# Performance work log

Measured on AMD Instinct MI355X. Metric: run time of the kernel, lower is better.

## Reference

```python
import jax, jax.numpy as jnp
from jax import lax
import numpy as np

SCORE_THRESH = 0.05
NMS_THRESH = 0.5
MAX_DET = 100
MIN_SIZE = 0.01
BBOX_CLIP = float(np.log(1000.0 / 16.0))
NEG = -1e10


def setup_inputs() -> dict:
    key = jax.random.key(0)
    ks = jax.random.split(key, 12)
    N, IN, REP, C = 2000, 256 * 7 * 7, 1024, 91
    box_features = jax.random.normal(ks[0], (N, IN), jnp.float32)
    x1 = jax.random.uniform(ks[1], (N,), jnp.float32, 0.0, 1000.0)
    y1 = jax.random.uniform(ks[2], (N,), jnp.float32, 0.0, 600.0)
    bw = jax.random.uniform(ks[3], (N,), jnp.float32, 16.0, 200.0)
    bh = jax.random.uniform(ks[4], (N,), jnp.float32, 16.0, 180.0)
    proposals = jnp.stack([x1, y1, x1 + bw, y1 + bh], axis=1)
    W1 = jax.random.normal(ks[5], (IN, REP), jnp.float32) * 0.01
    b1 = jnp.zeros((REP,), jnp.float32)
    W2 = jax.random.normal(ks[6], (REP, REP), jnp.float32) * 0.03
    b2 = jnp.zeros((REP,), jnp.float32)
    Wc = jax.random.normal(ks[7], (REP, C), jnp.float32) * 0.1
    bc = jax.random.normal(ks[8], (C,), jnp.float32) * 0.5
    Wr = jax.random.normal(ks[9], (REP, 4 * C), jnp.float32) * 0.01
    br = jnp.zeros((4 * C,), jnp.float32)
    return dict(box_features=box_features, proposals=proposals,
                W1=W1, b1=b1, W2=W2, b2=b2, Wc=Wc, bc=bc, Wr=Wr, br=br,
                image_h=800, image_w=1216)


def _nms(boxes, scores):
    """Greedy NMS with fixed trip count; scores already masked to NEG for invalid."""
    M = boxes.shape[0]
    areas = (boxes[:, 2] - boxes[:, 0]) * (boxes[:, 3] - boxes[:, 1])
    idxs = jnp.arange(M)

    def step(sm, _):
        i = jnp.argmax(sm)
        valid = sm[i] > NEG * 0.5
        b = boxes[i]
        xx1 = jnp.maximum(b[0], boxes[:, 0]); yy1 = jnp.maximum(b[1], boxes[:, 1])
        xx2 = jnp.minimum(b[2], boxes[:, 2]); yy2 = jnp.minimum(b[3], boxes[:, 3])
        inter = jnp.clip(xx2 - xx1, 0.0) * jnp.clip(yy2 - yy1, 0.0)
        iou = inter / (areas[i] + areas - inter + 1e-9)
        suppress = (iou > NMS_THRESH) | (idxs == i)
        sm = jnp.where(valid, jnp.where(suppress, NEG, sm), sm)
        return sm, jnp.where(valid, i, -1)

    _, keep = lax.scan(step, scores, None, length=MAX_DET)
    return keep  # [MAX_DET] int, -1 for padding


def reference(box_features, proposals, W1, b1, W2, b2, Wc, bc, Wr, br, image_h, image_w):
    N = box_features.shape[0]
    C = Wc.shape[1]
    # box head MLP (Linear+ReLU x2) and predictors
    h = jax.nn.relu(box_features @ W1 + b1)
    h = jax.nn.relu(h @ W2 + b2)
    class_logits = h @ Wc + bc                      # [N, C]
    box_reg = (h @ Wr + br).reshape(N, C, 4)        # [N, C, 4]
    # box decode (weights 10,10,5,5) against proposals
    pw = proposals[:, 2] - proposals[:, 0]
    ph = proposals[:, 3] - proposals[:, 1]
    pcx = proposals[:, 0] + 0.5 * pw
    pcy = proposals[:, 1] + 0.5 * ph
    dx = box_reg[..., 0] / 10.0
    dy = box_reg[..., 1] / 10.0
    dw = jnp.minimum(box_reg[..., 2] / 5.0, BBOX_CLIP)
    dh = jnp.minimum(box_reg[..., 3] / 5.0, BBOX_CLIP)
    cx = dx * pw[:, None] + pcx[:, None]
    cy = dy * ph[:, None] + pcy[:, None]
    w = jnp.exp(dw) * pw[:, None]
    hh = jnp.exp(dh) * ph[:, None]
    boxes = jnp.stack([cx - 0.5 * w, cy - 0.5 * hh, cx + 0.5 * w, cy + 0.5 * hh], axis=-1)
    scores = jax.nn.softmax(class_logits, axis=-1)
    # clip to image
    Wim = jnp.float32(image_w); Him = jnp.float32(image_h)
    boxes = jnp.stack([jnp.clip(boxes[..., 0], 0.0, Wim),
                       jnp.clip(boxes[..., 1], 0.0, Him),
                       jnp.clip(boxes[..., 2], 0.0, Wim),
                       jnp.clip(boxes[..., 3], 0.0, Him)], axis=-1)
    # drop background class, flatten to [N*(C-1)]
    boxes = boxes[:, 1:].reshape(-1, 4)
    scores = scores[:, 1:].reshape(-1)
    labels = jnp.broadcast_to(jnp.arange(1, C, dtype=jnp.int32), (N, C - 1)).reshape(-1)
    # score threshold + remove small boxes (as masking, static shapes)
    bw = boxes[:, 2] - boxes[:, 0]
    bh = boxes[:, 3] - boxes[:, 1]
    valid = (scores > SCORE_THRESH) & (bw >= MIN_SIZE) & (bh >= MIN_SIZE)
    sm = jnp.where(valid, scores, NEG)
    # class-aware (batched) NMS via per-class coordinate offsets
    off = labels.astype(boxes.dtype) * (jnp.maximum(Wim, Him) + 1.0)
    keep = _nms(boxes + off[:, None], sm)
    mask = keep >= 0
    idx = jnp.maximum(keep, 0)
    out_boxes = jnp.take(boxes, idx, axis=0) * mask[:, None]
    out_scores = jnp.take(scores, idx) * mask
    out_labels = jnp.take(labels, idx) * mask.astype(jnp.int32)
    return out_boxes, out_scores, out_labels
```

## Files before the change

kernel.cpp:

```cpp
#include <hip/hip_runtime.h>

#define CPC 2000
#define SPC 100
#define NCLS 90
#define TM 128
#define TN 128
#define TKK 16

typedef __attribute__((ext_vector_type(8))) short bf16x8;
typedef __attribute__((ext_vector_type(4))) float f32x4;
typedef __attribute__((ext_vector_type(4))) unsigned short u16x4;

__device__ __forceinline__ unsigned short f2bf_rne(float f) {
    unsigned u = __float_as_uint(f);
    return (unsigned short)((u + 0x7FFFu + ((u >> 16) & 1u)) >> 16);
}
__device__ __forceinline__ unsigned short f2bf_trunc(float f) {
    return (unsigned short)(__float_as_uint(f) >> 16);
}
__device__ __forceinline__ float bfhi_f32(float f) {
    return __uint_as_float(__float_as_uint(f) & 0xFFFF0000u);
}
__device__ __forceinline__ void async_load16(const void* g, void* l) {
    __builtin_amdgcn_global_load_lds((const __attribute__((address_space(1))) unsigned int*)g,
                                     (__attribute__((address_space(3))) unsigned int*)l, 16, 0, 0);
}
__device__ __forceinline__ int swz(int c) { return c ^ ((c >> 3) & 3); }

__global__ __launch_bounds__(256) void split_transpose(
    const float* __restrict__ W, unsigned short* __restrict__ Thi,
    unsigned short* __restrict__ Tlo, int K, int N)
{
    __shared__ float tile[64][33];
    const int kt = blockIdx.x * 64, nt = blockIdx.y * 32;
    const int tx = threadIdx.x & 31, ty = threadIdx.x >> 5;
#pragma unroll
    for (int j = 0; j < 8; ++j) {
        int k = kt + ty + j * 8, n = nt + tx;
        tile[ty + j * 8][tx] = (k < K && n < N) ? W[(size_t)k * N + n] : 0.f;
    }
    __syncthreads();
#pragma unroll
    for (int j = 0; j < 4; ++j) {
        int n = nt + ty + j * 8;
        int k = kt + tx * 2;
        if (n < N && k < K) {
            float f0 = tile[tx * 2][ty + j * 8];
            float f1 = tile[tx * 2 + 1][ty + j * 8];
            unsigned hi = (unsigned)f2bf_trunc(f0) | ((unsigned)f2bf_trunc(f1) << 16);
            unsigned lo = (unsigned)f2bf_rne(f0 - bfhi_f32(f0))
                        | ((unsigned)f2bf_rne(f1 - bfhi_f32(f1)) << 16);
            *reinterpret_cast<unsigned*>(&Thi[(size_t)n * K + k]) = hi;
            *reinterpret_cast<unsigned*>(&Tlo[(size_t)n * K + k]) = lo;
        }
    }
}

__global__ __launch_bounds__(256) void split_transpose2(
    const float* __restrict__ Wa, const float* __restrict__ Wb, int Na, int Nb,
    unsigned short* __restrict__ Thi, unsigned short* __restrict__ Tlo, int K)
{
    const int N = Na + Nb;
    __shared__ float tile[64][33];
    const int kt = blockIdx.x * 64, nt = blockIdx.y * 32;
    const int tx = threadIdx.x & 31, ty = threadIdx.x >> 5;
#pragma unroll
    for (int j = 0; j < 8; ++j) {
        int k = kt + ty + j * 8, n = nt + tx;
        float v = 0.f;
        if (k < K && n < N)
            v = (n < Na) ? Wa[(size_t)k * Na + n] : Wb[(size_t)k * Nb + (n - Na)];
        tile[ty + j * 8][tx] = v;
    }
    __syncthreads();
#pragma unroll
    for (int j = 0; j < 4; ++j) {
        int n = nt + ty + j * 8;
        int k = kt + tx * 2;
        if (n < N && k < K) {
            float f0 = tile[tx * 2][ty + j * 8];
            float f1 = tile[tx * 2 + 1][ty + j * 8];
            unsigned hi = (unsigned)f2bf_trunc(f0) | ((unsigned)f2bf_trunc(f1) << 16);
            unsigned lo = (unsigned)f2bf_rne(f0 - bfhi_f32(f0))
                        | ((unsigned)f2bf_rne(f1 - bfhi_f32(f1)) << 16);
            *reinterpret_cast<unsigned*>(&Thi[(size_t)n * K + k]) = hi;
            *reinterpret_cast<unsigned*>(&Tlo[(size_t)n * K + k]) = lo;
        }
    }
}

__global__ __launch_bounds__(256, 6) void gemm_bf16x3_f32a(
    const float* __restrict__ A, const unsigned short* __restrict__ Bhi,
    const unsigned short* __restrict__ Blo, float* __restrict__ C,
    int M, int N, int K, int klen)
{
    __shared__ unsigned short Ah[2048], Al[2048], Bh[4096], Bl[4096];
    const int tid = threadIdx.x;
    const int wv = tid >> 6, ln = tid & 63;
    const int q = ln >> 4, lm = ln & 15;
    const int m0 = blockIdx.y * 64, n0 = blockIdx.x * 128;
    const int k0 = blockIdx.z * klen;
    int k1 = k0 + klen; if (k1 > K) k1 = K;
    const int bcol_t = wv * 32;

    f32x4 acc[4][2];
#pragma unroll
    for (int i = 0; i < 4; ++i)
#pragma unroll
        for (int j = 0; j < 2; ++j) acc[i][j] = (f32x4)0.f;

    int gr = m0 + (tid >> 2); if (gr >= M) gr = M - 1;
    const float* Arow = A + (size_t)gr * K + (tid & 3) * 8;
    const int apc = swz(tid);

    unsigned bsrc[2];
#pragma unroll
    for (int i = 0; i < 2; ++i) {
        int s = i * 256 + tid;
        int gn = n0 + (s >> 2); if (gn >= N) gn = N - 1;
        int qe = (s & 3) ^ ((s >> 3) & 3);
        bsrc[i] = (unsigned)gn * (unsigned)K + (unsigned)(qe * 8);
    }

    for (int kt = k0; kt < k1; kt += 32) {
#pragma unroll
        for (int i = 0; i < 2; ++i) {
            async_load16(Bhi + bsrc[i] + kt, &Bh[(i * 256 + wv * 64) * 8]);
            async_load16(Blo + bsrc[i] + kt, &Bl[(i * 256 + wv * 64) * 8]);
        }
        float4 v0 = *reinterpret_cast<const float4*>(Arow + kt);
        float4 v1 = *reinterpret_cast<const float4*>(Arow + kt + 4);
        float f[8] = {v0.x, v0.y, v0.z, v0.w, v1.x, v1.y, v1.z, v1.w};
        bf16x8 hi, lo;
#pragma unroll
        for (int e = 0; e < 8; ++e) {
            hi[e] = (short)f2bf_trunc(f[e]);
            lo[e] = (short)f2bf_rne(f[e] - bfhi_f32(f[e]));
        }
        *(bf16x8*)&Ah[apc * 8] = hi;
        *(bf16x8*)&Al[apc * 8] = lo;
        __syncthreads();

        bf16x8 afh[4], afl[4], bfh[2], bfl[2];
#pragma unroll
        for (int mi = 0; mi < 4; ++mi) {
            int p = swz((mi * 16 + lm) * 4 + q);
            afh[mi] = *(const bf16x8*)&Ah[p * 8];
            afl[mi] = *(const bf16x8*)&Al[p * 8];
        }
#pragma unroll
        for (int ni = 0; ni < 2; ++ni) {
            int p = swz((bcol_t + ni * 16 + lm) * 4 + q);
            bfh[ni] = *(const bf16x8*)&Bh[p * 8];
            bfl[ni] = *(const bf16x8*)&Bl[p * 8];
        }
#pragma unroll
        for (int mi = 0; mi < 4; ++mi)
#pragma unroll
            for (int ni = 0; ni < 2; ++ni) {
                acc[mi][ni] = __builtin_amdgcn_mfma_f32_16x16x32_bf16(afh[mi], bfh[ni], acc[mi][ni], 0, 0, 0);
                acc[mi][ni] = __builtin_amdgcn_mfma_f32_16x16x32_bf16(afl[mi], bfh[ni], acc[mi][ni], 0, 0, 0);
                acc[mi][ni] = __builtin_amdgcn_mfma_f32_16x16x32_bf16(afh[mi], bfl[ni], acc[mi][ni], 0, 0, 0);
            }
        __syncthreads();
    }

    float* Cz = C + (size_t)blockIdx.z * (size_t)M * (size_t)N;
#pragma unroll
    for (int mi = 0; mi < 4; ++mi)
#pragma unroll
        for (int ni = 0; ni < 2; ++ni)
#pragma unroll
            for (int ri = 0; ri < 4; ++ri) {
                int rr = m0 + mi * 16 + q * 4 + ri;
                int cc = n0 + bcol_t + ni * 16 + lm;
                if (rr < M && cc < N) Cz[(size_t)rr * N + cc] = acc[mi][ni][ri];
            }
}

__global__ __launch_bounds__(256, 6) void gemm_bf16x3_sa(
    const unsigned short* __restrict__ Ahi_g, const unsigned short* __restrict__ Alo_g,
    const unsigned short* __restrict__ Bhi, const unsigned short* __restrict__ Blo,
    float* __restrict__ C, int M, int N, int K, int klen)
{
    __shared__ unsigned short Ah[2048], Al[2048], Bh[4096], Bl[4096];
    const int tid = threadIdx.x;
    const int wv = tid >> 6, ln = tid & 63;
    const int q = ln >> 4, lm = ln & 15;
    const int m0 = blockIdx.y * 64, n0 = blockIdx.x * 128;
    const int k0 = blockIdx.z * klen;
    int k1 = k0 + klen; if (k1 > K) k1 = K;
    const int bcol_t = wv * 32;

    f32x4 acc[4][2];
#pragma unroll
    for (int i = 0; i < 4; ++i)
#pragma unroll
        for (int j = 0; j < 2; ++j) acc[i][j] = (f32x4)0.f;

    int agr = m0 + (tid >> 2); if (agr >= M) agr = M - 1;
    const unsigned asrc = (unsigned)agr * (unsigned)K
                        + (unsigned)(((tid & 3) ^ ((tid >> 3) & 3)) * 8);

    unsigned bsrc[2];
#pragma unroll
    for (int i = 0; i < 2; ++i) {
        int s = i * 256 + tid;
        int gn = n0 + (s >> 2); if (gn >= N) gn = N - 1;
        int qe = (s & 3) ^ ((s >> 3) & 3);
        bsrc[i] = (unsigned)gn * (unsigned)K + (unsigned)(qe * 8);
    }

    for (int kt = k0; kt < k1; kt += 32) {
        async_load16(Ahi_g + asrc + kt, &Ah[(wv * 64) * 8]);
        async_load16(Alo_g + asrc + kt, &Al[(wv * 64) * 8]);
#pragma unroll
        for (int i = 0; i < 2; ++i) {
            async_load16(Bhi + bsrc[i] + kt, &Bh[(i * 256 + wv * 64) * 8]);
            async_load16(Blo + bsrc[i] + kt, &Bl[(i * 256 + wv * 64) * 8]);
        }
        __syncthreads();

        bf16x8 afh[4], afl[4], bfh[2], bfl[2];
#pragma unroll
        for (int mi = 0; mi < 4; ++mi) {
            int p = swz((mi * 16 + lm) * 4 + q);
            afh[mi] = *(const bf16x8*)&Ah[p * 8];
            afl[mi] = *(const bf16x8*)&Al[p * 8];
        }
#pragma unroll
        for (int ni = 0; ni < 2; ++ni) {
            int p = swz((bcol_t + ni * 16 + lm) * 4 + q);
            bfh[ni] = *(const bf16x8*)&Bh[p * 8];
            bfl[ni] = *(const bf16x8*)&Bl[p * 8];
        }
#pragma unroll
        for (int mi = 0; mi < 4; ++mi)
#pragma unroll
            for (int ni = 0; ni < 2; ++ni) {
                acc[mi][ni] = __builtin_amdgcn_mfma_f32_16x16x32_bf16(afh[mi], bfh[ni], acc[mi][ni], 0, 0, 0);
                acc[mi][ni] = __builtin_amdgcn_mfma_f32_16x16x32_bf16(afl[mi], bfh[ni], acc[mi][ni], 0, 0, 0);
                acc[mi][ni] = __builtin_amdgcn_mfma_f32_16x16x32_bf16(afh[mi], bfl[ni], acc[mi][ni], 0, 0, 0);
            }
        __syncthreads();
    }

    float* Cz = C + (size_t)blockIdx.z * (size_t)M * (size_t)N;
#pragma unroll
    for (int mi = 0; mi < 4; ++mi)
#pragma unroll
        for (int ni = 0; ni < 2; ++ni)
#pragma unroll
            for (int ri = 0; ri < 4; ++ri) {
                int rr = m0 + mi * 16 + q * 4 + ri;
                int cc = n0 + bcol_t + ni * 16 + lm;
                if (rr < M && cc < N) Cz[(size_t)rr * N + cc] = acc[mi][ni][ri];
            }
}

__global__ __launch_bounds__(256) void gemm_f32(
    const float* __restrict__ A, const float* __restrict__ B,
    const float* __restrict__ bias, float* __restrict__ C,
    int M, int N, int K, int ksplit, int relu)
{
    __shared__ float As[TKK][TM + 4];
    __shared__ float Bs[TKK][TN + 4];
    const int tid = threadIdx.x;
    const int tx = tid & 15, ty = tid >> 4;
    const int m0 = blockIdx.y * TM, n0 = blockIdx.x * TN;
    const int z = blockIdx.z;
    const int kstart = z * ksplit;
    const int kend = (kstart + ksplit < K) ? (kstart + ksplit) : K;
    float* Cz = C + (size_t)z * (size_t)M * (size_t)N;
    const bool nvec = ((N & 3) == 0);

    float acc[8][8];
#pragma unroll
    for (int i = 0; i < 8; ++i)
#pragma unroll
        for (int j = 0; j < 8; ++j) acc[i][j] = 0.f;

    for (int kt = kstart; kt < kend; kt += TKK) {
#pragma unroll
        for (int l = 0; l < 2; ++l) {
            int idx = tid + l * 256;
            int rr = idx >> 2, kq = idx & 3;
            float4 v = make_float4(0.f, 0.f, 0.f, 0.f);
            int grr = m0 + rr;
            if (grr < M)
                v = *reinterpret_cast<const float4*>(A + (size_t)grr * K + kt + (kq << 2));
            As[(kq << 2) + 0][rr] = v.x;
            As[(kq << 2) + 1][rr] = v.y;
            As[(kq << 2) + 2][rr] = v.z;
            As[(kq << 2) + 3][rr] = v.w;
        }
#pragma unroll
        for (int l = 0; l < 2; ++l) {
            int idx = tid + l * 256;
            int kk = idx >> 5, nq = idx & 31;
            int gn = n0 + (nq << 2);
            const float* bp = B + (size_t)(kt + kk) * N + gn;
            float4 v;
            if (nvec && gn + 3 < N) {
                v = *reinterpret_cast<const float4*>(bp);
            } else {
                v.x = (gn + 0 < N) ? bp[0] : 0.f;
                v.y = (gn + 1 < N) ? bp[1] : 0.f;
                v.z = (gn + 2 < N) ? bp[2] : 0.f;
                v.w = (gn + 3 < N) ? bp[3] : 0.f;
            }
            *reinterpret_cast<float4*>(&Bs[kk][nq << 2]) = v;
        }
        __syncthreads();
#pragma unroll
        for (int kk = 0; kk < TKK; ++kk) {
            float a[8], b[8];
            *reinterpret_cast<float4*>(&a[0]) = *reinterpret_cast<const float4*>(&As[kk][ty * 8]);
            *reinterpret_cast<float4*>(&a[4]) = *reinterpret_cast<const float4*>(&As[kk][ty * 8 + 4]);
            *reinterpret_cast<float4*>(&b[0]) = *reinterpret_cast<const float4*>(&Bs[kk][tx * 4]);
            *reinterpret_cast<float4*>(&b[4]) = *reinterpret_cast<const float4*>(&Bs[kk][64 + tx * 4]);
#pragma unroll
            for (int i = 0; i < 8; ++i)
#pragma unroll
                for (int j = 0; j < 8; ++j)
                    acc[i][j] = fmaf(a[i], b[j], acc[i][j]);
        }
        __syncthreads();
    }
#pragma unroll
    for (int i = 0; i < 8; ++i) {
        int grr = m0 + ty * 8 + i;
        if (grr >= M) continue;
#pragma unroll
        for (int j = 0; j < 8; ++j) {
            int gc = n0 + ((j < 4) ? (tx * 4 + j) : (64 + tx * 4 + (j - 4)));
            if (gc >= N) continue;
            float v = acc[i][j];
            if (bias) v += bias[gc];
            if (relu) v = fmaxf(v, 0.f);
            Cz[(size_t)grr * N + gc] = v;
        }
    }
}

__global__ void combine_bias_act(const float* __restrict__ P, const float* __restrict__ bias,
                                 float* __restrict__ H, int total, int N, int nsplit,
                                 int pstride, int relu)
{
    int i = blockIdx.x * blockDim.x + threadIdx.x;
    if (i >= total) return;
    float s = P[i];
    for (int j = 1; j < nsplit; ++j) s += P[i + (size_t)j * (size_t)pstride];
    s += bias[i % N];
    if (relu) s = fmaxf(s, 0.f);
    H[i] = s;
}

__global__ void combine_bias_split(const float* __restrict__ P, const float* __restrict__ bias,
                                   unsigned short* __restrict__ Hhi, unsigned short* __restrict__ Hlo,
                                   int total, int N, int nsplit, int pstride, int relu)
{
    int i = (blockIdx.x * blockDim.x + threadIdx.x) * 4;
    if (i >= total) return;
    float4 s = *reinterpret_cast<const float4*>(P + i);
    for (int j = 1; j < nsplit; ++j) {
        float4 p = *reinterpret_cast<const float4*>(P + i + (size_t)j * (size_t)pstride);
        s.x += p.x; s.y += p.y; s.z += p.z; s.w += p.w;
    }
    const float4 b = *reinterpret_cast<const float4*>(bias + (i % N));
    s.x += b.x; s.y += b.y; s.z += b.z; s.w += b.w;
    if (relu) {
        s.x = fmaxf(s.x, 0.f); s.y = fmaxf(s.y, 0.f);
        s.z = fmaxf(s.z, 0.f); s.w = fmaxf(s.w, 0.f);
    }
    u16x4 hi = { f2bf_trunc(s.x), f2bf_trunc(s.y), f2bf_trunc(s.z), f2bf_trunc(s.w) };
    u16x4 lo = { f2bf_rne(s.x - bfhi_f32(s.x)), f2bf_rne(s.y - bfhi_f32(s.y)),
                 f2bf_rne(s.z - bfhi_f32(s.z)), f2bf_rne(s.w - bfhi_f32(s.w)) };
    *reinterpret_cast<u16x4*>(&Hhi[i]) = hi;
    *reinterpret_cast<u16x4*>(&Hlo[i]) = lo;
}

__global__ void combine_head(const float* __restrict__ P, const float* __restrict__ bc,
                             const float* __restrict__ br, float* __restrict__ H,
                             int total, int nsplit, int pstride)
{
    int i = (blockIdx.x * blockDim.x + threadIdx.x) * 4;
    if (i >= total) return;
    float4 s = *reinterpret_cast<const float4*>(P + i);
    for (int j = 1; j < nsplit; ++j) {
        float4 p = *reinterpret_cast<const float4*>(P + i + (size_t)j * (size_t)pstride);
        s.x += p.x; s.y += p.y; s.z += p.z; s.w += p.w;
    }
    float sv[4] = {s.x, s.y, s.z, s.w};
#pragma unroll
    for (int e = 0; e < 4; ++e) {
        int col = (i + e) % 455;
        sv[e] += (col < 91) ? bc[col] : br[col - 91];
    }
    *reinterpret_cast<float4*>(&H[i]) = make_float4(sv[0], sv[1], sv[2], sv[3]);
}

__device__ __forceinline__ float scalar_dim(const int* p)
{
    int iv = *p;
    return (iv > 0 && iv < (1 << 20)) ? (float)iv : *reinterpret_cast<const float*>(p);
}

__global__ __launch_bounds__(128) void decode_compact(
    const float* __restrict__ logits, int lstr, const float* __restrict__ breg, int bstr,
    const float4* __restrict__ proposals, const int* __restrict__ ihp,
    const int* __restrict__ iwp,
    float4* __restrict__ cbox, float* __restrict__ cscore, int* __restrict__ cn,
    int* __restrict__ ccnt)
{
    const int n = blockIdx.x;
    const int c = threadIdx.x;
    __shared__ float sl[91];
    __shared__ float red[128];
    if (c < 91) sl[c] = logits[(size_t)n * lstr + c];
    __syncthreads();
    red[c] = (c < 91) ? sl[c] : -3.0e38f;
    __syncthreads();
#pragma unroll
    for (int s = 64; s > 0; s >>= 1) {
        if (c < s) red[c] = fmaxf(red[c], red[c + s]);
        __syncthreads();
    }
    const float s_max = red[0];
    __syncthreads();
    red[c] = (c < 91) ? expf(sl[c] - s_max) : 0.f;
    __syncthreads();
#pragma unroll
    for (int s = 64; s > 0; s >>= 1) {
        if (c < s) red[c] += red[c + s];
        __syncthreads();
    }
    const float s_sum = red[0];
    if (c < 1 || c >= 91) return;

    const float score = expf(sl[c] - s_max) / s_sum;
    const float Wim = scalar_dim(iwp), Him = scalar_dim(ihp);
    float4 p = proposals[n];
    float pw = p.z - p.x, ph = p.w - p.y;
    float pcx = p.x + 0.5f * pw, pcy = p.y + 0.5f * ph;
    const float* r4 = breg + (size_t)n * bstr + c * 4;
    float dxv = r4[0] / 10.f, dyv = r4[1] / 10.f;
    const float BCLIP = 4.135166556742356f;
    float dwv = fminf(r4[2] / 5.f, BCLIP);
    float dhv = fminf(r4[3] / 5.f, BCLIP);
    float cx = dxv * pw + pcx, cy = dyv * ph + pcy;
    float w = expf(dwv) * pw, hh = expf(dhv) * ph;
    float x1 = cx - 0.5f * w, y1 = cy - 0.5f * hh;
    float x2 = cx + 0.5f * w, y2 = cy + 0.5f * hh;
    x1 = fminf(fmaxf(x1, 0.f), Wim);
    y1 = fminf(fmaxf(y1, 0.f), Him);
    x2 = fminf(fmaxf(x2, 0.f), Wim);
    y2 = fminf(fmaxf(y2, 0.f), Him);
    float bw = x2 - x1, bh = y2 - y1;
    if (score > 0.05f && bw >= 0.01f && bh >= 0.01f) {
        int cls = c - 1;
        int pos = atomicAdd(&ccnt[cls], 1);
        if (pos < CPC) {
            cbox[cls * CPC + pos] = make_float4(x1, y1, x2, y2);
            cscore[cls * CPC + pos] = score;
            cn[cls * CPC + pos] = n;
        }
    }
}

__global__ __launch_bounds__(256) void nms_class(
    const float4* __restrict__ cbox, const float* __restrict__ cscore,
    const int* __restrict__ cn, const int* __restrict__ ccnt,
    float4* __restrict__ sbox, float* __restrict__ sscore,
    unsigned long long* __restrict__ skey, int* __restrict__ scnt)
{
    const int cls = blockIdx.x;
    const int tid = threadIdx.x;
    int cnt = ccnt[cls]; if (cnt > CPC) cnt = CPC;

    __shared__ float4 cb[CPC];
    __shared__ unsigned long long keys[CPC];
    __shared__ unsigned long long red[4];
    __shared__ float4 selsh;
    __shared__ int selidx_sh;

    for (int i = tid; i < cnt; i += 256) {
        cb[i] = cbox[cls * CPC + i];
        unsigned int sb = __float_as_uint(cscore[cls * CPC + i]);
        sb ^= (sb >> 31) ? 0xFFFFFFFFu : 0x80000000u;
        unsigned int flat = (unsigned)cn[cls * CPC + i] * 90u + (unsigned)cls;
        keys[i] = ((unsigned long long)sb << 32) | (unsigned long long)(0xFFFFFFFFu - flat);
    }
    __syncthreads();

    int sel = 0;
    while (sel < SPC) {
        unsigned long long best = 0ull;
        for (int i = tid; i < cnt; i += 256) {
            unsigned long long k = keys[i];
            if (k > best) best = k;
        }
#pragma unroll
        for (int d = 32; d >= 1; d >>= 1) {
            unsigned long long o = __shfl_down(best, d, 64);
            if (o > best) best = o;
        }
        if ((tid & 63) == 0) red[tid >> 6] = best;
        __syncthreads();
        unsigned long long gbest = red[0];
        if (red[1] > gbest) gbest = red[1];
        if (red[2] > gbest) gbest = red[2];
        if (red[3] > gbest) gbest = red[3];
        if (gbest == 0ull) break;
        for (int i = tid; i < cnt; i += 256)
            if (keys[i] == gbest) { selsh = cb[i]; selidx_sh = i; }
        __syncthreads();
        float4 s = selsh;
        const int si = selidx_sh;
        const float sa = (s.z - s.x) * (s.w - s.y);
        if (tid == 0) {
            sbox[cls * SPC + sel] = s;
            unsigned int sb = (unsigned int)(gbest >> 32);
            sb ^= (sb >> 31) ? 0x80000000u : 0xFFFFFFFFu;
            sscore[cls * SPC + sel] = __uint_as_float(sb);
            skey[cls * SPC + sel] = gbest;
        }
        for (int i = tid; i < cnt; i += 256) {
            float4 b = cb[i];
            float xx1 = fmaxf(s.x, b.x), yy1 = fmaxf(s.y, b.y);
            float xx2 = fminf(s.z, b.z), yy2 = fminf(s.w, b.w);
            float inter = fmaxf(xx2 - xx1, 0.f) * fmaxf(yy2 - yy1, 0.f);
            float area = (b.z - b.x) * (b.w - b.y);
            if (3.f * inter > sa + area + 1e-9f || i == si) keys[i] = 0ull;
        }
        ++sel;
        __syncthreads();
    }
    if (tid == 0) scnt[cls] = sel;
}

__global__ __launch_bounds__(128) void nms_merge(
    const float4* __restrict__ sbox, const float* __restrict__ sscore,
    const unsigned long long* __restrict__ skey, const int* __restrict__ scnt,
    float* __restrict__ out)
{
    const int tid = threadIdx.x;
    __shared__ int head[NCLS];
    __shared__ unsigned long long red[2];
    __shared__ int selc_sh;
    if (tid < NCLS) head[tid] = 0;
    __syncthreads();

    for (int k = 0; k < 100; ++k) {
        unsigned long long key = 0ull;
        if (tid < NCLS && head[tid] < scnt[tid]) key = skey[tid * SPC + head[tid]];
        unsigned long long mykey = key;
#pragma unroll
        for (int d = 32; d >= 1; d >>= 1) {
            unsigned long long o = __shfl_down(key, d, 64);
            if (o > key) key = o;
        }
        if ((tid & 63) == 0) red[tid >> 6] = key;
        if (tid == 0) selc_sh = -1;
        __syncthreads();
        unsigned long long gbest = red[0] > red[1] ? red[0] : red[1];
        if (gbest != 0ull && mykey == gbest) selc_sh = tid;
        __syncthreads();
        const int c = selc_sh;
        if (tid == 0) {
            if (c >= 0) {
                int h = head[c];
                float4 b = sbox[c * SPC + h];
                out[k * 4 + 0] = b.x; out[k * 4 + 1] = b.y;
                out[k * 4 + 2] = b.z; out[k * 4 + 3] = b.w;
                out[400 + k] = sscore[c * SPC + h];
                out[500 + k] = (float)(c + 1);
            } else {
                out[k * 4 + 0] = 0.f; out[k * 4 + 1] = 0.f;
                out[k * 4 + 2] = 0.f; out[k * 4 + 3] = 0.f;
                out[400 + k] = 0.f; out[500 + k] = 0.f;
            }
        }
        if (c >= 0 && tid == c) head[c]++;
        __syncthreads();
    }
}

extern "C" void kernel_launch(void* const* d_in, const int* in_sizes, int n_in,
                              void* d_out, int out_size, void* d_ws, size_t ws_size,
                              hipStream_t stream)
{
    const float* bf    = (const float*)d_in[0];
    const float* props = (const float*)d_in[1];
    const float* W1    = (const float*)d_in[2];
    const float* b1    = (const float*)d_in[3];
    const float* W2    = (const float*)d_in[4];
    const float* b2    = (const float*)d_in[5];
    const float* Wc    = (const float*)d_in[6];
    const float* bc    = (const float*)d_in[7];
    const float* Wr    = (const float*)d_in[8];
    const float* br    = (const float*)d_in[9];
    const int*   ihp   = (const int*)d_in[10];
    const int*   iwp   = (const int*)d_in[11];
    float* ws  = (float*)d_ws;
    float* out = (float*)d_out;

    const size_t MN   = 2000ull * 1024ull;
    const size_t NLOG = 2000ull * 91ull;
    const size_t NREG = 2000ull * 364ull;
    const size_t NHEAD = 2000ull * 455ull;
    const size_t ws_floats = ws_size / 4;

    const size_t BT1F = 1024ull * 12544ull / 2;
    const size_t WT2F = 1024ull * 1024ull / 2;
    const size_t WHF  = 455ull * 1024ull / 2;
    const size_t NMSF = (size_t)NCLS * CPC * 6 + (size_t)NCLS * SPC * 7 + 256;
    const size_t PF   = 4 * MN;
    const size_t NEED = 2 * BT1F + 2 * WT2F + 2 * WHF + 2 * MN + NHEAD + NMSF + PF + 64;

    if (ws_floats >= NEED) {
        unsigned short* BT1hi = (unsigned short*)ws;
        unsigned short* BT1lo = (unsigned short*)(ws + BT1F);
        unsigned short* WT2hi = (unsigned short*)(ws + 2 * BT1F);
        unsigned short* WT2lo = (unsigned short*)(ws + 2 * BT1F + WT2F);
        unsigned short* WHhi  = (unsigned short*)(ws + 2 * BT1F + 2 * WT2F);
        unsigned short* WHlo  = (unsigned short*)(ws + 2 * BT1F + 2 * WT2F + WHF);
        float* T = ws + 2 * BT1F + 2 * WT2F + 2 * WHF;

        float* H1   = T;
        float* P1   = T + MN;
        float* P2   = T + MN;
        float* H2   = T + 6 * MN;
        float* P3   = T;
        float* HEAD = T + 7 * MN;
        float* CBOX   = T;
        float* CSCORE = CBOX + (size_t)NCLS * CPC * 4;
        int*   CN     = (int*)(CSCORE + (size_t)NCLS * CPC);
        float* SBOX   = (float*)(CN + (size_t)NCLS * CPC);
        float* SSCORE = SBOX + (size_t)NCLS * SPC * 4;
        unsigned long long* SKEY = (unsigned long long*)(SSCORE + (size_t)NCLS * SPC);
        int*   CCNT = (int*)(SKEY + (size_t)NCLS * SPC);
        int*   SCNT = CCNT + NCLS;

        unsigned short* H1hi = (unsigned short*)H1;
        unsigned short* H1lo = H1hi + MN;
        unsigned short* H2hi = (unsigned short*)H2;
        unsigned short* H2lo = H2hi + MN;

        split_transpose<<<dim3(196, 32), 256, 0, stream>>>(W1, BT1hi, BT1lo, 12544, 1024);
        split_transpose<<<dim3(16, 32), 256, 0, stream>>>(W2, WT2hi, WT2lo, 1024, 1024);
        split_transpose2<<<dim3(16, 15), 256, 0, stream>>>(Wc, Wr, 91, 364, WHhi, WHlo, 1024);
        gemm_bf16x3_f32a<<<dim3(8, 32, 6), 256, 0, stream>>>(bf, BT1hi, BT1lo, P1,
                                                             2000, 1024, 12544, 2112);
        combine_bias_split<<<(int)(MN / 4 / 256), 256, 0, stream>>>(P1, b1, H1hi, H1lo,
                                                             (int)MN, 1024, 6, (int)MN, 1);
        gemm_bf16x3_sa<<<dim3(8, 32, 5), 256, 0, stream>>>(H1hi, H1lo, WT2hi, WT2lo, P2,
                                                           2000, 1024, 1024, 224);
        combine_bias_split<<<(int)(MN / 4 / 256), 256, 0, stream>>>(P2, b2, H2hi, H2lo,
                                                             (int)MN, 1024, 5, (int)MN, 1);
        gemm_bf16x3_sa<<<dim3(4, 32, 6), 256, 0, stream>>>(H2hi, H2lo, WHhi, WHlo, P3,
                                                           2000, 455, 1024, 192);
        combine_head<<<(int)((NHEAD / 4 + 255) / 256), 256, 0, stream>>>(P3, bc, br, HEAD,
                                                             (int)NHEAD, 6, (int)NHEAD);
        hipMemsetAsync(CCNT, 0, 2 * NCLS * sizeof(int), stream);
        decode_compact<<<2000, 128, 0, stream>>>(HEAD, 455, HEAD + 91, 455,
                                                 (const float4*)props, ihp, iwp,
                                                 (float4*)CBOX, CSCORE, CN, CCNT);
        nms_class<<<NCLS, 256, 0, stream>>>((const float4*)CBOX, CSCORE, CN, CCNT,
                                            (float4*)SBOX, SSCORE, SKEY, SCNT);
        nms_merge<<<1, 128, 0, stream>>>((const float4*)SBOX, SSCORE, SKEY, SCNT, out);
        return;
    }

    const size_t NMSF2 = (size_t)NCLS * CPC * 6 + (size_t)NCLS * SPC * 7 + 256;
    const size_t TAILF = 2 * MN + NLOG + NREG + NMSF2;
    int z1 = 2;
    if (ws_floats >= TAILF + 8 * MN) z1 = 8;
    else if (ws_floats >= TAILF + 4 * MN) z1 = 4;
    const size_t REUSE = (size_t)z1 * MN;
    int zh = (REUSE >= 8 * NREG) ? 8 : 4;

    float* P      = ws;
    float* H1     = P + REUSE;
    float* H2     = H1 + MN;
    float* LOG    = H2 + MN;
    float* BREG   = LOG + NLOG;
    float* CBOX   = BREG + NREG;
    float* CSCORE = CBOX + (size_t)NCLS * CPC * 4;
    int*   CN     = (int*)(CSCORE + (size_t)NCLS * CPC);
    float* SBOX   = (float*)(CN + (size_t)NCLS * CPC);
    float* SSCORE = SBOX + (size_t)NCLS * SPC * 4;
    unsigned long long* SKEY = (unsigned long long*)(SSCORE + (size_t)NCLS * SPC);
    int*   CCNT   = (int*)(SKEY + (size_t)NCLS * SPC);
    int*   SCNT   = CCNT + NCLS;

    gemm_f32<<<dim3(8, 16, z1), 256, 0, stream>>>(bf, W1, nullptr, P,
                                                  2000, 1024, 12544, 12544 / z1, 0);
    combine_bias_act<<<(int)((MN + 255) / 256), 256, 0, stream>>>(P, b1, H1,
                                                  (int)MN, 1024, z1, (int)MN, 1);
    gemm_f32<<<dim3(8, 16, 4), 256, 0, stream>>>(H1, W2, nullptr, P,
                                                 2000, 1024, 1024, 256, 0);
    combine_bias_act<<<(int)((MN + 255) / 256), 256, 0, stream>>>(P, b2, H2,
                                                 (int)MN, 1024, 4, (int)MN, 1);
    gemm_f32<<<dim3(1, 16, zh), 256, 0, stream>>>(H2, Wc, nullptr, P,
                                                  2000, 91, 1024, 1024 / zh, 0);
    combine_bias_act<<<(int)((NLOG + 255) / 256), 256, 0, stream>>>(P, bc, LOG,
                                                  (int)NLOG, 91, zh, (int)NLOG, 0);
    gemm_f32<<<dim3(3, 16, zh), 256, 0, stream>>>(H2, Wr, nullptr, P,
                                                  2000, 364, 1024, 1024 / zh, 0);
    combine_bias_act<<<(int)((NREG + 255) / 256), 256, 0, stream>>>(P, br, BREG,
                                                  (int)NREG, 364, zh, (int)NREG, 0);
    hipMemsetAsync(CCNT, 0, 2 * NCLS * sizeof(int), stream);
    decode_compact<<<2000, 128, 0, stream>>>(LOG, 91, BREG, 364,
                                             (const float4*)props, ihp, iwp,
                                             (float4*)CBOX, CSCORE, CN, CCNT);
    nms_class<<<NCLS, 256, 0, stream>>>((const float4*)CBOX, CSCORE, CN, CCNT,
                                        (float4*)SBOX, SSCORE, SKEY, SCNT);
    nms_merge<<<1, 128, 0, stream>>>((const float4*)SBOX, SSCORE, SKEY, SCNT, out);
}
```

Before: 830.6 us.

## Remap GEMM workgroups across XCDs, retune split-K, and separate partial-sum buffer

Adds an XCD-aware remap of linear block IDs so that neighbouring tiles, which share A and B panels, land on the same XCD and reuse its L2. It also lowers the launch-bounds occupancy hint from 6 to 4 and changes the split-K factors: 4 for the first two GEMMs and 8 for the head GEMM. The workspace is rearranged so partial sums go to a dedicated buffer P instead of aliasing the activation region. The aim is less L2 and HBM traffic in the large first GEMM and less partial-sum reduction work, at the cost of fewer blocks in flight for the first two GEMMs and a different register budget per block.

Measured after the change: 734.7 us. 1.13x faster.

```diff
diff --git a/kernel.cpp b/kernel.cpp
--- a/kernel.cpp
+++ b/kernel.cpp
@@ -26,6 +26,19 @@
                                      (__attribute__((address_space(3))) unsigned int*)l, 16, 0, 0);
 }
 __device__ __forceinline__ int swz(int c) { return c ^ ((c >> 3) & 3); }
+
+__device__ __forceinline__ void xcd_remap(unsigned& bx, unsigned& by, unsigned& bz)
+{
+    const unsigned nx = gridDim.x, ny = gridDim.y;
+    const unsigned nwg = nx * ny * gridDim.z;
+    unsigned lin = blockIdx.x + nx * (blockIdx.y + ny * blockIdx.z);
+    if ((nwg & 7u) == 0u)
+        lin = (lin & 7u) * (nwg >> 3) + (lin >> 3);
+    bx = lin % nx;
+    unsigned rem = lin / nx;
+    by = rem % ny;
+    bz = rem / ny;
+}
 
 __global__ __launch_bounds__(256) void split_transpose(
     const float* __restrict__ W, unsigned short* __restrict__ Thi,
@@ -89,17 +102,19 @@
     }
 }
 
-__global__ __launch_bounds__(256, 6) void gemm_bf16x3_f32a(
+__global__ __launch_bounds__(256, 4) void gemm_bf16x3_f32a(
     const float* __restrict__ A, const unsigned short* __restrict__ Bhi,
     const unsigned short* __restrict__ Blo, float* __restrict__ C,
     int M, int N, int K, int klen)
 {
     __shared__ unsigned short Ah[2048], Al[2048], Bh[4096], Bl[4096];
+    unsigned bxu, byu, bzu;
+    xcd_remap(bxu, byu, bzu);
     const int tid = threadIdx.x;
     const int wv = tid >> 6, ln = tid & 63;
     const int q = ln >> 4, lm = ln & 15;
-    const int m0 = blockIdx.y * 64, n0 = blockIdx.x * 128;
-    const int k0 = blockIdx.z * klen;
+    const int m0 = byu * 64, n0 = bxu * 128;
+    const int k0 = bzu * klen;
     int k1 = k0 + klen; if (k1 > K) k1 = K;
     const int bcol_t = wv * 32;
 
@@ -165,7 +180,7 @@
         __syncthreads();
     }
 
-    float* Cz = C + (size_t)blockIdx.z * (size_t)M * (size_t)N;
+    float* Cz = C + (size_t)bzu * (size_t)M * (size_t)N;
 #pragma unroll
     for (int mi = 0; mi < 4; ++mi)
 #pragma unroll
@@ -178,17 +193,19 @@
             }
 }
 
-__global__ __launch_bounds__(256, 6) void gemm_bf16x3_sa(
+__global__ __launch_bounds__(256, 4) void gemm_bf16x3_sa(
     const unsigned short* __restrict__ Ahi_g, const unsigned short* __restrict__ Alo_g,
     const unsigned short* __restrict__ Bhi, const unsigned short* __restrict__ Blo,
     float* __restrict__ C, int M, int N, int K, int klen)
 {
     __shared__ unsigned short Ah[2048], Al[2048], Bh[4096], Bl[4096];
+    unsigned bxu, byu, bzu;
+    xcd_remap(bxu, byu, bzu);
     const int tid = threadIdx.x;
     const int wv = tid >> 6, ln = tid & 63;
     const int q = ln >> 4, lm = ln & 15;
-    const int m0 = blockIdx.y * 64, n0 = blockIdx.x * 128;
-    const int k0 = blockIdx.z * klen;
+    const int m0 = byu * 64, n0 = bxu * 128;
+    const int k0 = bzu * klen;
     int k1 = k0 + klen; if (k1 > K) k1 = K;
     const int bcol_t = wv * 32;
 
@@ -245,7 +262,7 @@
         __syncthreads();
     }
 
-    float* Cz = C + (size_t)blockIdx.z * (size_t)M * (size_t)N;
+    float* Cz = C + (size_t)bzu * (size_t)M * (size_t)N;
 #pragma unroll
     for (int mi = 0; mi < 4; ++mi)
 #pragma unroll
@@ -625,15 +642,10 @@
         unsigned short* WT2lo = (unsigned short*)(ws + 2 * BT1F + WT2F);
         unsigned short* WHhi  = (unsigned short*)(ws + 2 * BT1F + 2 * WT2F);
         unsigned short* WHlo  = (unsigned short*)(ws + 2 * BT1F + 2 * WT2F + WHF);
-        float* T = ws + 2 * BT1F + 2 * WT2F + 2 * WHF;
-
-        float* H1   = T;
-        float* P1   = T + MN;
-        float* P2   = T + MN;
-        float* H2   = T + 6 * MN;
-        float* P3   = T;
-        float* HEAD = T + 7 * MN;
-        float* CBOX   = T;
+        float* H1   = ws + 2 * BT1F + 2 * WT2F + 2 * WHF;
+        float* H2   = H1 + MN;
+        float* HEAD = H2 + MN;
+        float* CBOX   = HEAD + NHEAD;
         float* CSCORE = CBOX + (size_t)NCLS * CPC * 4;
         int*   CN     = (int*)(CSCORE + (size_t)NCLS * CPC);
         float* SBOX   = (float*)(CN + (size_t)NCLS * CPC);
@@ -641,6 +653,7 @@
         unsigned long long* SKEY = (unsigned long long*)(SSCORE + (size_t)NCLS * SPC);
         int*   CCNT = (int*)(SKEY + (size_t)NCLS * SPC);
         int*   SCNT = CCNT + NCLS;
+        float* P = (float*)(SCNT + NCLS + 64);
 
         unsigned short* H1hi = (unsigned short*)H1;
         unsigned short* H1lo = H1hi + MN;
@@ -650,18 +663,18 @@
         split_transpose<<<dim3(196, 32), 256, 0, stream>>>(W1, BT1hi, BT1lo, 12544, 1024);
         split_transpose<<<dim3(16, 32), 256, 0, stream>>>(W2, WT2hi, WT2lo, 1024, 1024);
         split_transpose2<<<dim3(16, 15), 256, 0, stream>>>(Wc, Wr, 91, 364, WHhi, WHlo, 1024);
-        gemm_bf16x3_f32a<<<dim3(8, 32, 6), 256, 0, stream>>>(bf, BT1hi, BT1lo, P1,
-                                                             2000, 1024, 12544, 2112);
-        combine_bias_split<<<(int)(MN / 4 / 256), 256, 0, stream>>>(P1, b1, H1hi, H1lo,
-                                                             (int)MN, 1024, 6, (int)MN, 1);
-        gemm_bf16x3_sa<<<dim3(8, 32, 5), 256, 0, stream>>>(H1hi, H1lo, WT2hi, WT2lo, P2,
-                                                           2000, 1024, 1024, 224);
-        combine_bias_split<<<(int)(MN / 4 / 256), 256, 0, stream>>>(P2, b2, H2hi, H2lo,
-                                                             (int)MN, 1024, 5, (int)MN, 1);
-        gemm_bf16x3_sa<<<dim3(4, 32, 6), 256, 0, stream>>>(H2hi, H2lo, WHhi, WHlo, P3,
-                                                           2000, 455, 1024, 192);
-        combine_head<<<(int)((NHEAD / 4 + 255) / 256), 256, 0, stream>>>(P3, bc, br, HEAD,
-                                                             (int)NHEAD, 6, (int)NHEAD);
+        gemm_bf16x3_f32a<<<dim3(8, 32, 4), 256, 0, stream>>>(bf, BT1hi, BT1lo, P,
+                                                             2000, 1024, 12544, 3136);
+        combine_bias_split<<<(int)(MN / 4 / 256), 256, 0, stream>>>(P, b1, H1hi, H1lo,
+                                                             (int)MN, 1024, 4, (int)MN, 1);
+        gemm_bf16x3_sa<<<dim3(8, 32, 4), 256, 0, stream>>>(H1hi, H1lo, WT2hi, WT2lo, P,
+                                                           2000, 1024, 1024, 256);
+        combine_bias_split<<<(int)(MN / 4 / 256), 256, 0, stream>>>(P, b2, H2hi, H2lo,
+                                                             (int)MN, 1024, 4, (int)MN, 1);
+        gemm_bf16x3_sa<<<dim3(4, 32, 8), 256, 0, stream>>>(H2hi, H2lo, WHhi, WHlo, P,
+                                                           2000, 455, 1024, 128);
+        combine_head<<<(int)((NHEAD / 4 + 255) / 256), 256, 0, stream>>>(P, bc, br, HEAD,
+                                                             (int)NHEAD, 8, (int)NHEAD);
         hipMemsetAsync(CCNT, 0, 2 * NCLS * sizeof(int), stream);
         decode_compact<<<2000, 128, 0, stream>>>(HEAD, 455, HEAD + 91, 455,
                                                  (const float4*)props, ihp, iwp,
```
